# Kernel tuning notes

Hardware: AMD Instinct MI355X
Metric: run time of the kernel (lower is better)

## Reference

```python
import jax, jax.numpy as jnp
import numpy as np

N = 50000
E = 800000
D_IN = 128
D_OUT = 128


def setup_inputs() -> dict:
    key = jax.random.key(0)
    k1, k2, k3 = jax.random.split(key, 3)
    seq = jax.random.normal(k1, (N, D_IN), dtype=jnp.float32)
    edge_index = jax.random.randint(k2, (2, E), 0, N, dtype=jnp.int32)
    # Glorot-ish init for the GCNConv linear weight [in, out]
    W = jax.random.normal(k3, (D_IN, D_OUT), dtype=jnp.float32) * (1.0 / np.sqrt(D_IN))
    b = jnp.zeros((D_OUT,), dtype=jnp.float32)
    prelu_w = jnp.full((1,), 0.25, dtype=jnp.float32)
    return {"seq": seq, "edge_index": edge_index, "W": W, "b": b, "prelu_w": prelu_w}


def reference(seq, edge_index, W, b, prelu_w):
    # GCNConv: linear transform, add self-loops, symmetric normalization,
    # scatter-add aggregation, bias; then PReLU activation.
    n = seq.shape[0]
    xW = seq @ W  # [N, D_OUT]

    # add self-loops
    loop = jnp.arange(n, dtype=edge_index.dtype)
    row = jnp.concatenate([edge_index[0], loop])  # source
    col = jnp.concatenate([edge_index[1], loop])  # target

    # degree of target nodes (edge weight = 1)
    deg = jax.ops.segment_sum(jnp.ones_like(col, dtype=xW.dtype), col, num_segments=n)
    dinv = jnp.where(deg > 0, jax.lax.rsqrt(deg), 0.0)
    norm = dinv[row] * dinv[col]  # [E+N]

    msg = xW[row] * norm[:, None]  # gather + scale
    out = jax.ops.segment_sum(msg, col, num_segments=n)  # scatter-add
    out = out + b

    # PReLU with single shared weight
    return jnp.where(out > 0, out, prelu_w[0] * out)
```

## Files before the change

### kernel.cpp

```cpp
#include <hip/hip_runtime.h>

constexpr int D = 128;
constexpr int CAP = 64;
constexpr int OVFCAP = 65536;

typedef __attribute__((ext_vector_type(8))) short short8;
typedef __attribute__((ext_vector_type(4))) float f32x4;

__device__ __forceinline__ unsigned short f2bf(float f) {
    unsigned u = __float_as_uint(f);
    u += 0x7fffu + ((u >> 16) & 1u);
    return (unsigned short)(u >> 16);
}

__global__ __launch_bounds__(256) void k_prep(const float* __restrict__ W,
                                              unsigned short* __restrict__ Wf) {
    int tid = blockIdx.x * 256 + threadIdx.x;
    int j  = tid & 7;
    int l  = (tid >> 3) & 63;
    int g  = tid >> 9;
    int kc = g >> 3, t = g & 7;
    int k  = kc * 32 + ((l >> 4) * 4) + (j & 3) + ((j >> 2) * 16);
    int c  = t * 16 + (l & 15);
    Wf[tid] = f2bf(W[k * D + c]);
}

__global__ __launch_bounds__(256) void k_place_gemm(
        const int* __restrict__ row, const int* __restrict__ col,
        int* __restrict__ deg, int* __restrict__ slots,
        int* __restrict__ ovfCnt, int2* __restrict__ ovf, int E,
        int gemmBlocks,
        const float* __restrict__ seq, const unsigned short* __restrict__ Wf,
        unsigned short* __restrict__ y16, int n) {
    int b = (int)blockIdx.x;
    int half = b >> 1;
    bool isGemm = ((b & 1) == 0) && (half < gemmBlocks);

    if (!isGemm) {
        int pIdx = (b < 2 * gemmBlocks) ? half : (b - gemmBlocks);
        int t = pIdx * 256 + threadIdx.x;
        int e = 2 * t;
        if (e + 1 < E) {
            int2 c2 = *(const int2*)(col + e);
            int2 r2 = *(const int2*)(row + e);
            int p0 = atomicAdd(&deg[c2.x], 1);
            int p1 = atomicAdd(&deg[c2.y], 1);
            if (p0 < CAP) slots[(size_t)c2.x * CAP + p0] = r2.x;
            else { int o = atomicAdd(ovfCnt, 1); if (o < OVFCAP) ovf[o] = make_int2(r2.x, c2.x); }
            if (p1 < CAP) slots[(size_t)c2.y * CAP + p1] = r2.y;
            else { int o = atomicAdd(ovfCnt, 1); if (o < OVFCAP) ovf[o] = make_int2(r2.y, c2.y); }
        } else if (e < E) {
            int c = col[e];
            int r = row[e];
            int p = atomicAdd(&deg[c], 1);
            if (p < CAP) slots[(size_t)c * CAP + p] = r;
            else { int o = atomicAdd(ovfCnt, 1); if (o < OVFCAP) ovf[o] = make_int2(r, c); }
        }
        return;
    }

    int w  = threadIdx.x >> 6;
    int l  = threadIdx.x & 63;
    int lr = l & 15;
    int lg = l >> 4;

    int row0 = half * 64;
    int m = row0 + w * 16 + lr;
    if (m >= n) m = n - 1;
    const float* sp = seq + (size_t)m * D;

    f32x4 acc[8];
    #pragma unroll
    for (int t = 0; t < 8; ++t) acc[t] = (f32x4){0.f, 0.f, 0.f, 0.f};

    const short8* WfB = (const short8*)Wf;

    #pragma unroll
    for (int kc = 0; kc < 4; ++kc) {
        int kb = kc * 32 + lg * 4;
        float4 lo = *(const float4*)(sp + kb);
        float4 hi = *(const float4*)(sp + kb + 16);
        short8 a;
        a[0] = (short)f2bf(lo.x); a[1] = (short)f2bf(lo.y);
        a[2] = (short)f2bf(lo.z); a[3] = (short)f2bf(lo.w);
        a[4] = (short)f2bf(hi.x); a[5] = (short)f2bf(hi.y);
        a[6] = (short)f2bf(hi.z); a[7] = (short)f2bf(hi.w);
        #pragma unroll
        for (int t = 0; t < 8; ++t) {
            short8 bf = WfB[(kc * 8 + t) * 64 + l];
            acc[t] = __builtin_amdgcn_mfma_f32_16x16x32_bf16(a, bf, acc[t], 0, 0, 0);
        }
    }

    #pragma unroll
    for (int i = 0; i < 4; ++i) {
        int g = row0 + w * 16 + lg * 4 + i;
        if (g < n) {
            unsigned short* yp = y16 + (size_t)g * D + lr;
            #pragma unroll
            for (int t = 0; t < 8; ++t) yp[t * 16] = f2bf(acc[t][i]);
        }
    }
}

__global__ __launch_bounds__(256) void k_agg(
        const int* __restrict__ slots, const int* __restrict__ deg,
        const int* __restrict__ ovfCnt, const int2* __restrict__ ovf,
        const unsigned short* __restrict__ y16,
        const float* __restrict__ b, const float* __restrict__ pw,
        float* __restrict__ out, int n) {
    int wid = (blockIdx.x * 256 + threadIdx.x) >> 6;
    if (wid >= n) return;
    int lane = threadIdx.x & 63;

    int cntf = deg[wid];
    int cnt = cntf < CAP ? cntf : CAP;
    float dc = rsqrtf((float)(cntf + 1));

    unsigned sv = *(const unsigned*)(y16 + (size_t)wid * D + 2 * lane);
    float ax0 = __uint_as_float(sv << 16) * dc;
    float ay0 = __uint_as_float(sv & 0xffff0000u) * dc;
    float ax1 = 0.f, ay1 = 0.f, ax2 = 0.f, ay2 = 0.f, ax3 = 0.f, ay3 = 0.f;
    float ax4 = 0.f, ay4 = 0.f, ax5 = 0.f, ay5 = 0.f, ax6 = 0.f, ay6 = 0.f;
    float ax7 = 0.f, ay7 = 0.f;

    int my = (lane < cnt) ? slots[(size_t)wid * CAP + lane] : 0;

    int k = 0;
    for (; k + 7 < cnt; k += 8) {
        int r0 = __shfl(my, k);
        int r1 = __shfl(my, k + 1);
        int r2 = __shfl(my, k + 2);
        int r3 = __shfl(my, k + 3);
        int r4 = __shfl(my, k + 4);
        int r5 = __shfl(my, k + 5);
        int r6 = __shfl(my, k + 6);
        int r7 = __shfl(my, k + 7);
        int g0 = deg[r0]; int g1 = deg[r1]; int g2 = deg[r2]; int g3 = deg[r3];
        int g4 = deg[r4]; int g5 = deg[r5]; int g6 = deg[r6]; int g7 = deg[r7];
        unsigned v0 = *(const unsigned*)(y16 + (size_t)r0 * D + 2 * lane);
        unsigned v1 = *(const unsigned*)(y16 + (size_t)r1 * D + 2 * lane);
        unsigned v2 = *(const unsigned*)(y16 + (size_t)r2 * D + 2 * lane);
        unsigned v3 = *(const unsigned*)(y16 + (size_t)r3 * D + 2 * lane);
        unsigned v4 = *(const unsigned*)(y16 + (size_t)r4 * D + 2 * lane);
        unsigned v5 = *(const unsigned*)(y16 + (size_t)r5 * D + 2 * lane);
        unsigned v6 = *(const unsigned*)(y16 + (size_t)r6 * D + 2 * lane);
        unsigned v7 = *(const unsigned*)(y16 + (size_t)r7 * D + 2 * lane);
        float dr0 = rsqrtf((float)(g0 + 1));
        float dr1 = rsqrtf((float)(g1 + 1));
        float dr2 = rsqrtf((float)(g2 + 1));
        float dr3 = rsqrtf((float)(g3 + 1));
        float dr4 = rsqrtf((float)(g4 + 1));
        float dr5 = rsqrtf((float)(g5 + 1));
        float dr6 = rsqrtf((float)(g6 + 1));
        float dr7 = rsqrtf((float)(g7 + 1));
        ax0 = fmaf(__uint_as_float(v0 << 16), dr0, ax0); ay0 = fmaf(__uint_as_float(v0 & 0xffff0000u), dr0, ay0);
        ax1 = fmaf(__uint_as_float(v1 << 16), dr1, ax1); ay1 = fmaf(__uint_as_float(v1 & 0xffff0000u), dr1, ay1);
        ax2 = fmaf(__uint_as_float(v2 << 16), dr2, ax2); ay2 = fmaf(__uint_as_float(v2 & 0xffff0000u), dr2, ay2);
        ax3 = fmaf(__uint_as_float(v3 << 16), dr3, ax3); ay3 = fmaf(__uint_as_float(v3 & 0xffff0000u), dr3, ay3);
        ax4 = fmaf(__uint_as_float(v4 << 16), dr4, ax4); ay4 = fmaf(__uint_as_float(v4 & 0xffff0000u), dr4, ay4);
        ax5 = fmaf(__uint_as_float(v5 << 16), dr5, ax5); ay5 = fmaf(__uint_as_float(v5 & 0xffff0000u), dr5, ay5);
        ax6 = fmaf(__uint_as_float(v6 << 16), dr6, ax6); ay6 = fmaf(__uint_as_float(v6 & 0xffff0000u), dr6, ay6);
        ax7 = fmaf(__uint_as_float(v7 << 16), dr7, ax7); ay7 = fmaf(__uint_as_float(v7 & 0xffff0000u), dr7, ay7);
    }
    for (; k < cnt; ++k) {
        int r = __shfl(my, k);
        float dr = rsqrtf((float)(deg[r] + 1));
        unsigned v = *(const unsigned*)(y16 + (size_t)r * D + 2 * lane);
        ax0 = fmaf(__uint_as_float(v << 16), dr, ax0);
        ay0 = fmaf(__uint_as_float(v & 0xffff0000u), dr, ay0);
    }

    if (cntf > CAP) {
        int m = *ovfCnt; if (m > OVFCAP) m = OVFCAP;
        for (int j = 0; j < m; ++j) {
            int2 pr = ovf[j];
            if (pr.y == wid) {
                float dr = rsqrtf((float)(deg[pr.x] + 1));
                unsigned v = *(const unsigned*)(y16 + (size_t)pr.x * D + 2 * lane);
                ax0 = fmaf(__uint_as_float(v << 16), dr, ax0);
                ay0 = fmaf(__uint_as_float(v & 0xffff0000u), dr, ay0);
            }
        }
    }

    float sx = ((ax0 + ax1) + (ax2 + ax3)) + ((ax4 + ax5) + (ax6 + ax7));
    float sy = ((ay0 + ay1) + (ay2 + ay3)) + ((ay4 + ay5) + (ay6 + ay7));

    float2 bb = *(const float2*)(b + 2 * lane);
    float p = pw[0];
    float vx = sx * dc + bb.x;
    float vy = sy * dc + bb.y;
    vx = vx > 0.f ? vx : p * vx;
    vy = vy > 0.f ? vy : p * vy;
    *(float2*)(out + (size_t)wid * D + 2 * lane) = make_float2(vx, vy);
}

extern "C" void kernel_launch(void* const* d_in, const int* in_sizes, int n_in,
                              void* d_out, int out_size, void* d_ws, size_t ws_size,
                              hipStream_t stream) {
    const float* seq = (const float*)d_in[0];
    const int*   ei  = (const int*)d_in[1];
    const float* W   = (const float*)d_in[2];
    const float* b   = (const float*)d_in[3];
    const float* pw  = (const float*)d_in[4];
    int n = in_sizes[0] / D;
    int E = in_sizes[1] / 2;

    float* out = (float*)d_out;

    auto align = [](size_t x) { return (x + 255) & ~(size_t)255; };
    char* p = (char*)d_ws;
    unsigned short* y16 = (unsigned short*)p; p += align((size_t)n * D * sizeof(unsigned short));
    int*  deg    = (int*)p;   size_t degBytes = align((size_t)n * sizeof(int)); p += degBytes;
    int*  ovfCnt = (int*)p;   p += 256;
    int2* ovf    = (int2*)p;  p += align((size_t)OVFCAP * sizeof(int2));
    int*  slots  = (int*)p;   p += align((size_t)n * CAP * sizeof(int));
    unsigned short* Wf = (unsigned short*)p; p += align((size_t)D * D * sizeof(unsigned short));

    hipMemsetAsync(deg, 0, degBytes + 256, stream);
    k_prep<<<64, 256, 0, stream>>>(W, Wf);

    int GB = (n + 63) / 64;
    int PB = (E + 511) / 512;
    k_place_gemm<<<GB + PB, 256, 0, stream>>>(
        ei, ei + E, deg, slots, ovfCnt, ovf, E, GB, seq, Wf, y16, n);

    k_agg<<<(unsigned)(((long long)n * 64 + 255) / 256), 256, 0, stream>>>(
        slots, deg, ovfCnt, ovf, y16, b, pw, out, n);
}
```

Baseline: 99.37 us.

## Prescale features by source-degree norm and pad degree counters to cache lines

Adds a k_scale pass that multiplies each bf16 row of xW by rsqrt(deg+1) ahead of aggregation. This removes the per-neighbour degree gather and rsqrt from k_agg, whose inner loop becomes plain adds. Degree counters are padded to 64-byte stride to cut atomic contention, each placement thread handles four edges with int4 loads, and CAP drops to 48. The cost is one extra kernel launch, an extra read-write pass over y16 with a second bf16 rounding, a larger memset, and possibly more overflow traffic.

```diff
diff --git a/kernel.cpp b/kernel.cpp
--- a/kernel.cpp
+++ b/kernel.cpp
@@ -1,7 +1,8 @@
 #include <hip/hip_runtime.h>
 
 constexpr int D = 128;
-constexpr int CAP = 64;
+constexpr int CAP = 48;
+constexpr int DPAD = 16;
 constexpr int OVFCAP = 65536;
 
 typedef __attribute__((ext_vector_type(8))) short short8;
@@ -27,7 +28,7 @@
 
 __global__ __launch_bounds__(256) void k_place_gemm(
         const int* __restrict__ row, const int* __restrict__ col,
-        int* __restrict__ deg, int* __restrict__ slots,
+        int* __restrict__ degP, int* __restrict__ slots,
         int* __restrict__ ovfCnt, int2* __restrict__ ovf, int E,
         int gemmBlocks,
         const float* __restrict__ seq, const unsigned short* __restrict__ Wf,
@@ -39,22 +40,33 @@
     if (!isGemm) {
         int pIdx = (b < 2 * gemmBlocks) ? half : (b - gemmBlocks);
         int t = pIdx * 256 + threadIdx.x;
-        int e = 2 * t;
-        if (e + 1 < E) {
-            int2 c2 = *(const int2*)(col + e);
-            int2 r2 = *(const int2*)(row + e);
-            int p0 = atomicAdd(&deg[c2.x], 1);
-            int p1 = atomicAdd(&deg[c2.y], 1);
-            if (p0 < CAP) slots[(size_t)c2.x * CAP + p0] = r2.x;
-            else { int o = atomicAdd(ovfCnt, 1); if (o < OVFCAP) ovf[o] = make_int2(r2.x, c2.x); }
-            if (p1 < CAP) slots[(size_t)c2.y * CAP + p1] = r2.y;
-            else { int o = atomicAdd(ovfCnt, 1); if (o < OVFCAP) ovf[o] = make_int2(r2.y, c2.y); }
-        } else if (e < E) {
-            int c = col[e];
-            int r = row[e];
-            int p = atomicAdd(&deg[c], 1);
-            if (p < CAP) slots[(size_t)c * CAP + p] = r;
-            else { int o = atomicAdd(ovfCnt, 1); if (o < OVFCAP) ovf[o] = make_int2(r, c); }
+        int e = 4 * t;
+        if (e + 3 < E) {
+            int4 c4 = *(const int4*)(col + e);
+            int4 r4 = *(const int4*)(row + e);
+            int p0 = atomicAdd(&degP[(size_t)c4.x * DPAD], 1);
+            int p1 = atomicAdd(&degP[(size_t)c4.y * DPAD], 1);
+            int p2 = atomicAdd(&degP[(size_t)c4.z * DPAD], 1);
+            int p3 = atomicAdd(&degP[(size_t)c4.w * DPAD], 1);
+            if (p0 < CAP) slots[(size_t)c4.x * CAP + p0] = r4.x;
+            else { int o = atomicAdd(ovfCnt, 1); if (o < OVFCAP) ovf[o] = make_int2(r4.x, c4.x); }
+            if (p1 < CAP) slots[(size_t)c4.y * CAP + p1] = r4.y;
+            else { int o = atomicAdd(ovfCnt, 1); if (o < OVFCAP) ovf[o] = make_int2(r4.y, c4.y); }
+            if (p2 < CAP) slots[(size_t)c4.z * CAP + p2] = r4.z;
+            else { int o = atomicAdd(ovfCnt, 1); if (o < OVFCAP) ovf[o] = make_int2(r4.z, c4.z); }
+            if (p3 < CAP) slots[(size_t)c4.w * CAP + p3] = r4.w;
+            else { int o = atomicAdd(ovfCnt, 1); if (o < OVFCAP) ovf[o] = make_int2(r4.w, c4.w); }
+        } else {
+            for (int j = 0; j < 4; ++j) {
+                int ej = e + j;
+                if (ej < E) {
+                    int c = col[ej];
+                    int r = row[ej];
+                    int p = atomicAdd(&degP[(size_t)c * DPAD], 1);
+                    if (p < CAP) slots[(size_t)c * CAP + p] = r;
+                    else { int o = atomicAdd(ovfCnt, 1); if (o < OVFCAP) ovf[o] = make_int2(r, c); }
+                }
+            }
         }
         return;
     }
@@ -103,8 +115,40 @@
     }
 }
 
+__global__ __launch_bounds__(256) void k_scale(unsigned short* __restrict__ y16,
+                                               const int* __restrict__ degP, int n) {
+    int tid = blockIdx.x * 256 + threadIdx.x;
+    int total = n * (D / 8);
+    if (tid >= total) return;
+    int g = tid >> 4;
+    float di = rsqrtf((float)(degP[(size_t)g * DPAD] + 1));
+    uint4 v = ((uint4*)y16)[tid];
+    unsigned r0, r1, r2, r3;
+    {
+        float lo = __uint_as_float(v.x << 16) * di;
+        float hi = __uint_as_float(v.x & 0xffff0000u) * di;
+        r0 = (unsigned)f2bf(lo) | ((unsigned)f2bf(hi) << 16);
+    }
+    {
+        float lo = __uint_as_float(v.y << 16) * di;
+        float hi = __uint_as_float(v.y & 0xffff0000u) * di;
+        r1 = (unsigned)f2bf(lo) | ((unsigned)f2bf(hi) << 16);
+    }
+    {
+        float lo = __uint_as_float(v.z << 16) * di;
+        float hi = __uint_as_float(v.z & 0xffff0000u) * di;
+        r2 = (unsigned)f2bf(lo) | ((unsigned)f2bf(hi) << 16);
+    }
+    {
+        float lo = __uint_as_float(v.w << 16) * di;
+        float hi = __uint_as_float(v.w & 0xffff0000u) * di;
+        r3 = (unsigned)f2bf(lo) | ((unsigned)f2bf(hi) << 16);
+    }
+    ((uint4*)y16)[tid] = make_uint4(r0, r1, r2, r3);
+}
+
 __global__ __launch_bounds__(256) void k_agg(
-        const int* __restrict__ slots, const int* __restrict__ deg,
+        const int* __restrict__ slots, const int* __restrict__ degP,
         const int* __restrict__ ovfCnt, const int2* __restrict__ ovf,
         const unsigned short* __restrict__ y16,
         const float* __restrict__ b, const float* __restrict__ pw,
@@ -113,13 +157,13 @@
     if (wid >= n) return;
     int lane = threadIdx.x & 63;
 
-    int cntf = deg[wid];
+    int cntf = degP[(size_t)wid * DPAD];
     int cnt = cntf < CAP ? cntf : CAP;
     float dc = rsqrtf((float)(cntf + 1));
 
     unsigned sv = *(const unsigned*)(y16 + (size_t)wid * D + 2 * lane);
-    float ax0 = __uint_as_float(sv << 16) * dc;
-    float ay0 = __uint_as_float(sv & 0xffff0000u) * dc;
+    float ax0 = __uint_as_float(sv << 16);
+    float ay0 = __uint_as_float(sv & 0xffff0000u);
     float ax1 = 0.f, ay1 = 0.f, ax2 = 0.f, ay2 = 0.f, ax3 = 0.f, ay3 = 0.f;
     float ax4 = 0.f, ay4 = 0.f, ax5 = 0.f, ay5 = 0.f, ax6 = 0.f, ay6 = 0.f;
     float ax7 = 0.f, ay7 = 0.f;
@@ -136,8 +180,6 @@
         int r5 = __shfl(my, k + 5);
         int r6 = __shfl(my, k + 6);
         int r7 = __shfl(my, k + 7);
-        int g0 = deg[r0]; int g1 = deg[r1]; int g2 = deg[r2]; int g3 = deg[r3];
-        int g4 = deg[r4]; int g5 = deg[r5]; int g6 = deg[r6]; int g7 = deg[r7];
         unsigned v0 = *(const unsigned*)(y16 + (size_t)r0 * D + 2 * lane);
         unsigned v1 = *(const unsigned*)(y16 + (size_t)r1 * D + 2 * lane);
         unsigned v2 = *(const unsigned*)(y16 + (size_t)r2 * D + 2 * lane);
@@ -146,29 +188,20 @@
         unsigned v5 = *(const unsigned*)(y16 + (size_t)r5 * D + 2 * lane);
         unsigned v6 = *(const unsigned*)(y16 + (size_t)r6 * D + 2 * lane);
         unsigned v7 = *(const unsigned*)(y16 + (size_t)r7 * D + 2 * lane);
-        float dr0 = rsqrtf((float)(g0 + 1));
-        float dr1 = rsqrtf((float)(g1 + 1));
-        float dr2 = rsqrtf((float)(g2 + 1));
-        float dr3 = rsqrtf((float)(g3 + 1));
-        float dr4 = rsqrtf((float)(g4 + 1));
-        float dr5 = rsqrtf((float)(g5 + 1));
-        float dr6 = rsqrtf((float)(g6 + 1));
-        float dr7 = rsqrtf((float)(g7 + 1));
-        ax0 = fmaf(__uint_as_float(v0 << 16), dr0, ax0); ay0 = fmaf(__uint_as_float(v0 & 0xffff0000u), dr0, ay0);
-        ax1 = fmaf(__uint_as_float(v1 << 16), dr1, ax1); ay1 = fmaf(__uint_as_float(v1 & 0xffff0000u), dr1, ay1);
-        ax2 = fmaf(__uint_as_float(v2 << 16), dr2, ax2); ay2 = fmaf(__uint_as_float(v2 & 0xffff0000u), dr2, ay2);
-        ax3 = fmaf(__uint_as_float(v3 << 16), dr3, ax3); ay3 = fmaf(__uint_as_float(v3 & 0xffff0000u), dr3, ay3);
-        ax4 = fmaf(__uint_as_float(v4 << 16), dr4, ax4); ay4 = fmaf(__uint_as_float(v4 & 0xffff0000u), dr4, ay4);
-        ax5 = fmaf(__uint_as_float(v5 << 16), dr5, ax5); ay5 = fmaf(__uint_as_float(v5 & 0xffff0000u), dr5, ay5);
-        ax6 = fmaf(__uint_as_float(v6 << 16), dr6, ax6); ay6 = fmaf(__uint_as_float(v6 & 0xffff0000u), dr6, ay6);
-        ax7 = fmaf(__uint_as_float(v7 << 16), dr7, ax7); ay7 = fmaf(__uint_as_float(v7 & 0xffff0000u), dr7, ay7);
+        ax0 += __uint_as_float(v0 << 16); ay0 += __uint_as_float(v0 & 0xffff0000u);
+        ax1 += __uint_as_float(v1 << 16); ay1 += __uint_as_float(v1 & 0xffff0000u);
+        ax2 += __uint_as_float(v2 << 16); ay2 += __uint_as_float(v2 & 0xffff0000u);
+        ax3 += __uint_as_float(v3 << 16); ay3 += __uint_as_float(v3 & 0xffff0000u);
+        ax4 += __uint_as_float(v4 << 16); ay4 += __uint_as_float(v4 & 0xffff0000u);
+        ax5 += __uint_as_float(v5 << 16); ay5 += __uint_as_float(v5 & 0xffff0000u);
+        ax6 += __uint_as_float(v6 << 16); ay6 += __uint_as_float(v6 & 0xffff0000u);
+        ax7 += __uint_as_float(v7 << 16); ay7 += __uint_as_float(v7 & 0xffff0000u);
     }
     for (; k < cnt; ++k) {
         int r = __shfl(my, k);
-        float dr = rsqrtf((float)(deg[r] + 1));
         unsigned v = *(const unsigned*)(y16 + (size_t)r * D + 2 * lane);
-        ax0 = fmaf(__uint_as_float(v << 16), dr, ax0);
-        ay0 = fmaf(__uint_as_float(v & 0xffff0000u), dr, ay0);
+        ax0 += __uint_as_float(v << 16);
+        ay0 += __uint_as_float(v & 0xffff0000u);
     }
 
     if (cntf > CAP) {
@@ -176,10 +209,9 @@
         for (int j = 0; j < m; ++j) {
             int2 pr = ovf[j];
             if (pr.y == wid) {
-                float dr = rsqrtf((float)(deg[pr.x] + 1));
                 unsigned v = *(const unsigned*)(y16 + (size_t)pr.x * D + 2 * lane);
-                ax0 = fmaf(__uint_as_float(v << 16), dr, ax0);
-                ay0 = fmaf(__uint_as_float(v & 0xffff0000u), dr, ay0);
+                ax0 += __uint_as_float(v << 16);
+                ay0 += __uint_as_float(v & 0xffff0000u);
             }
         }
     }
@@ -212,20 +244,23 @@
     auto align = [](size_t x) { return (x + 255) & ~(size_t)255; };
     char* p = (char*)d_ws;
     unsigned short* y16 = (unsigned short*)p; p += align((size_t)n * D * sizeof(unsigned short));
-    int*  deg    = (int*)p;   size_t degBytes = align((size_t)n * sizeof(int)); p += degBytes;
+    int*  degP   = (int*)p;   size_t degBytes = align((size_t)n * DPAD * sizeof(int)); p += degBytes;
     int*  ovfCnt = (int*)p;   p += 256;
     int2* ovf    = (int2*)p;  p += align((size_t)OVFCAP * sizeof(int2));
     int*  slots  = (int*)p;   p += align((size_t)n * CAP * sizeof(int));
     unsigned short* Wf = (unsigned short*)p; p += align((size_t)D * D * sizeof(unsigned short));
 
-    hipMemsetAsync(deg, 0, degBytes + 256, stream);
+    hipMemsetAsync(degP, 0, degBytes + 256, stream);
     k_prep<<<64, 256, 0, stream>>>(W, Wf);
 
     int GB = (n + 63) / 64;
-    int PB = (E + 511) / 512;
+    int PB = (E + 1023) / 1024;
     k_place_gemm<<<GB + PB, 256, 0, stream>>>(
-        ei, ei + E, deg, slots, ovfCnt, ovf, E, GB, seq, Wf, y16, n);
+        ei, ei + E, degP, slots, ovfCnt, ovf, E, GB, seq, Wf, y16, n);
+
+    int scaleTotal = n * (D / 8);
+    k_scale<<<(scaleTotal + 255) / 256, 256, 0, stream>>>(y16, degP, n);
 
     k_agg<<<(unsigned)(((long long)n * 64 + 255) / 256), 256, 0, stream>>>(
-        slots, deg, ovfCnt, ovf, y16, b, pw, out, n);
-}
+        slots, degP, ovfCnt, ovf, y16, b, pw, out, n);
+}
```

Result: faster. 89.41 us (-10.0%).

## Pad degree counters, precompute dinv array, fuse zeroing into prep, shrink slot cap

Applied to the files above, without the earlier changes.

The degree counters are padded to 64-byte stride so atomics from different nodes no longer contend on shared cache lines. A new small kernel precomputes rsqrt of each degree into a dense float array, which the aggregation gathers instead of the padded counters followed by rsqrt. The memset is replaced by zeroing inside the weight-prep kernel, edge indices are read with nontemporal loads, and CAP drops from 64 to 48 to shrink the slot buffer. The costs are an extra kernel launch, a larger degree array to zero, and more edges going to the slow overflow path for high-degree nodes.

```diff
diff --git a/kernel.cpp b/kernel.cpp
--- a/kernel.cpp
+++ b/kernel.cpp
@@ -1,7 +1,8 @@
 #include <hip/hip_runtime.h>
 
 constexpr int D = 128;
-constexpr int CAP = 64;
+constexpr int CAP = 48;
+constexpr int DPAD = 16;
 constexpr int OVFCAP = 65536;
 
 typedef __attribute__((ext_vector_type(8))) short short8;
@@ -14,8 +15,11 @@
 }
 
 __global__ __launch_bounds__(256) void k_prep(const float* __restrict__ W,
-                                              unsigned short* __restrict__ Wf) {
+                                              unsigned short* __restrict__ Wf,
+                                              uint4* __restrict__ zbase, int zcnt4) {
     int tid = blockIdx.x * 256 + threadIdx.x;
+    for (int i = tid; i < zcnt4; i += 16384) zbase[i] = make_uint4(0u, 0u, 0u, 0u);
+
     int j  = tid & 7;
     int l  = (tid >> 3) & 63;
     int g  = tid >> 9;
@@ -27,7 +31,7 @@
 
 __global__ __launch_bounds__(256) void k_place_gemm(
         const int* __restrict__ row, const int* __restrict__ col,
-        int* __restrict__ deg, int* __restrict__ slots,
+        int* __restrict__ degP, int* __restrict__ slots,
         int* __restrict__ ovfCnt, int2* __restrict__ ovf, int E,
         int gemmBlocks,
         const float* __restrict__ seq, const unsigned short* __restrict__ Wf,
@@ -41,18 +45,20 @@
         int t = pIdx * 256 + threadIdx.x;
         int e = 2 * t;
         if (e + 1 < E) {
-            int2 c2 = *(const int2*)(col + e);
-            int2 r2 = *(const int2*)(row + e);
-            int p0 = atomicAdd(&deg[c2.x], 1);
-            int p1 = atomicAdd(&deg[c2.y], 1);
-            if (p0 < CAP) slots[(size_t)c2.x * CAP + p0] = r2.x;
-            else { int o = atomicAdd(ovfCnt, 1); if (o < OVFCAP) ovf[o] = make_int2(r2.x, c2.x); }
-            if (p1 < CAP) slots[(size_t)c2.y * CAP + p1] = r2.y;
-            else { int o = atomicAdd(ovfCnt, 1); if (o < OVFCAP) ovf[o] = make_int2(r2.y, c2.y); }
+            unsigned long long cc = __builtin_nontemporal_load((const unsigned long long*)(col + e));
+            unsigned long long rr = __builtin_nontemporal_load((const unsigned long long*)(row + e));
+            int c0 = (int)(cc & 0xffffffffu), c1 = (int)(cc >> 32);
+            int r0 = (int)(rr & 0xffffffffu), r1 = (int)(rr >> 32);
+            int p0 = atomicAdd(&degP[(size_t)c0 * DPAD], 1);
+            int p1 = atomicAdd(&degP[(size_t)c1 * DPAD], 1);
+            if (p0 < CAP) slots[(size_t)c0 * CAP + p0] = r0;
+            else { int o = atomicAdd(ovfCnt, 1); if (o < OVFCAP) ovf[o] = make_int2(r0, c0); }
+            if (p1 < CAP) slots[(size_t)c1 * CAP + p1] = r1;
+            else { int o = atomicAdd(ovfCnt, 1); if (o < OVFCAP) ovf[o] = make_int2(r1, c1); }
         } else if (e < E) {
             int c = col[e];
             int r = row[e];
-            int p = atomicAdd(&deg[c], 1);
+            int p = atomicAdd(&degP[(size_t)c * DPAD], 1);
             if (p < CAP) slots[(size_t)c * CAP + p] = r;
             else { int o = atomicAdd(ovfCnt, 1); if (o < OVFCAP) ovf[o] = make_int2(r, c); }
         }
@@ -103,8 +109,15 @@
     }
 }
 
+__global__ __launch_bounds__(256) void k_dinv(const int* __restrict__ degP,
+                                              float* __restrict__ dinv, int n) {
+    int i = blockIdx.x * 256 + threadIdx.x;
+    if (i < n) dinv[i] = rsqrtf((float)(degP[(size_t)i * DPAD] + 1));
+}
+
 __global__ __launch_bounds__(256) void k_agg(
-        const int* __restrict__ slots, const int* __restrict__ deg,
+        const int* __restrict__ slots, const int* __restrict__ degP,
+        const float* __restrict__ dinv,
         const int* __restrict__ ovfCnt, const int2* __restrict__ ovf,
         const unsigned short* __restrict__ y16,
         const float* __restrict__ b, const float* __restrict__ pw,
@@ -113,9 +126,9 @@
     if (wid >= n) return;
     int lane = threadIdx.x & 63;
 
-    int cntf = deg[wid];
+    int cntf = degP[(size_t)wid * DPAD];
     int cnt = cntf < CAP ? cntf : CAP;
-    float dc = rsqrtf((float)(cntf + 1));
+    float dc = dinv[wid];
 
     unsigned sv = *(const unsigned*)(y16 + (size_t)wid * D + 2 * lane);
     float ax0 = __uint_as_float(sv << 16) * dc;
@@ -136,8 +149,8 @@
         int r5 = __shfl(my, k + 5);
         int r6 = __shfl(my, k + 6);
         int r7 = __shfl(my, k + 7);
-        int g0 = deg[r0]; int g1 = deg[r1]; int g2 = deg[r2]; int g3 = deg[r3];
-        int g4 = deg[r4]; int g5 = deg[r5]; int g6 = deg[r6]; int g7 = deg[r7];
+        float d0 = dinv[r0]; float d1 = dinv[r1]; float d2 = dinv[r2]; float d3 = dinv[r3];
+        float d4 = dinv[r4]; float d5 = dinv[r5]; float d6 = dinv[r6]; float d7 = dinv[r7];
         unsigned v0 = *(const unsigned*)(y16 + (size_t)r0 * D + 2 * lane);
         unsigned v1 = *(const unsigned*)(y16 + (size_t)r1 * D + 2 * lane);
         unsigned v2 = *(const unsigned*)(y16 + (size_t)r2 * D + 2 * lane);
@@ -146,26 +159,18 @@
         unsigned v5 = *(const unsigned*)(y16 + (size_t)r5 * D + 2 * lane);
         unsigned v6 = *(const unsigned*)(y16 + (size_t)r6 * D + 2 * lane);
         unsigned v7 = *(const unsigned*)(y16 + (size_t)r7 * D + 2 * lane);
-        float dr0 = rsqrtf((float)(g0 + 1));
-        float dr1 = rsqrtf((float)(g1 + 1));
-        float dr2 = rsqrtf((float)(g2 + 1));
-        float dr3 = rsqrtf((float)(g3 + 1));
-        float dr4 = rsqrtf((float)(g4 + 1));
-        float dr5 = rsqrtf((float)(g5 + 1));
-        float dr6 = rsqrtf((float)(g6 + 1));
-        float dr7 = rsqrtf((float)(g7 + 1));
-        ax0 = fmaf(__uint_as_float(v0 << 16), dr0, ax0); ay0 = fmaf(__uint_as_float(v0 & 0xffff0000u), dr0, ay0);
-        ax1 = fmaf(__uint_as_float(v1 << 16), dr1, ax1); ay1 = fmaf(__uint_as_float(v1 & 0xffff0000u), dr1, ay1);
-        ax2 = fmaf(__uint_as_float(v2 << 16), dr2, ax2); ay2 = fmaf(__uint_as_float(v2 & 0xffff0000u), dr2, ay2);
-        ax3 = fmaf(__uint_as_float(v3 << 16), dr3, ax3); ay3 = fmaf(__uint_as_float(v3 & 0xffff0000u), dr3, ay3);
-        ax4 = fmaf(__uint_as_float(v4 << 16), dr4, ax4); ay4 = fmaf(__uint_as_float(v4 & 0xffff0000u), dr4, ay4);
-        ax5 = fmaf(__uint_as_float(v5 << 16), dr5, ax5); ay5 = fmaf(__uint_as_float(v5 & 0xffff0000u), dr5, ay5);
-        ax6 = fmaf(__uint_as_float(v6 << 16), dr6, ax6); ay6 = fmaf(__uint_as_float(v6 & 0xffff0000u), dr6, ay6);
-        ax7 = fmaf(__uint_as_float(v7 << 16), dr7, ax7); ay7 = fmaf(__uint_as_float(v7 & 0xffff0000u), dr7, ay7);
+        ax0 = fmaf(__uint_as_float(v0 << 16), d0, ax0); ay0 = fmaf(__uint_as_float(v0 & 0xffff0000u), d0, ay0);
+        ax1 = fmaf(__uint_as_float(v1 << 16), d1, ax1); ay1 = fmaf(__uint_as_float(v1 & 0xffff0000u), d1, ay1);
+        ax2 = fmaf(__uint_as_float(v2 << 16), d2, ax2); ay2 = fmaf(__uint_as_float(v2 & 0xffff0000u), d2, ay2);
+        ax3 = fmaf(__uint_as_float(v3 << 16), d3, ax3); ay3 = fmaf(__uint_as_float(v3 & 0xffff0000u), d3, ay3);
+        ax4 = fmaf(__uint_as_float(v4 << 16), d4, ax4); ay4 = fmaf(__uint_as_float(v4 & 0xffff0000u), d4, ay4);
+        ax5 = fmaf(__uint_as_float(v5 << 16), d5, ax5); ay5 = fmaf(__uint_as_float(v5 & 0xffff0000u), d5, ay5);
+        ax6 = fmaf(__uint_as_float(v6 << 16), d6, ax6); ay6 = fmaf(__uint_as_float(v6 & 0xffff0000u), d6, ay6);
+        ax7 = fmaf(__uint_as_float(v7 << 16), d7, ax7); ay7 = fmaf(__uint_as_float(v7 & 0xffff0000u), d7, ay7);
     }
     for (; k < cnt; ++k) {
         int r = __shfl(my, k);
-        float dr = rsqrtf((float)(deg[r] + 1));
+        float dr = dinv[r];
         unsigned v = *(const unsigned*)(y16 + (size_t)r * D + 2 * lane);
         ax0 = fmaf(__uint_as_float(v << 16), dr, ax0);
         ay0 = fmaf(__uint_as_float(v & 0xffff0000u), dr, ay0);
@@ -176,7 +181,7 @@
         for (int j = 0; j < m; ++j) {
             int2 pr = ovf[j];
             if (pr.y == wid) {
-                float dr = rsqrtf((float)(deg[pr.x] + 1));
+                float dr = dinv[pr.x];
                 unsigned v = *(const unsigned*)(y16 + (size_t)pr.x * D + 2 * lane);
                 ax0 = fmaf(__uint_as_float(v << 16), dr, ax0);
                 ay0 = fmaf(__uint_as_float(v & 0xffff0000u), dr, ay0);
@@ -212,20 +217,23 @@
     auto align = [](size_t x) { return (x + 255) & ~(size_t)255; };
     char* p = (char*)d_ws;
     unsigned short* y16 = (unsigned short*)p; p += align((size_t)n * D * sizeof(unsigned short));
-    int*  deg    = (int*)p;   size_t degBytes = align((size_t)n * sizeof(int)); p += degBytes;
+    int*  degP   = (int*)p;   size_t degBytes = align((size_t)n * DPAD * sizeof(int)); p += degBytes;
     int*  ovfCnt = (int*)p;   p += 256;
     int2* ovf    = (int2*)p;  p += align((size_t)OVFCAP * sizeof(int2));
     int*  slots  = (int*)p;   p += align((size_t)n * CAP * sizeof(int));
     unsigned short* Wf = (unsigned short*)p; p += align((size_t)D * D * sizeof(unsigned short));
-
-    hipMemsetAsync(deg, 0, degBytes + 256, stream);
-    k_prep<<<64, 256, 0, stream>>>(W, Wf);
+    float* dinv  = (float*)p; p += align((size_t)n * sizeof(float));
+
+    int zcnt4 = (int)((degBytes + 256) / 16);
+    k_prep<<<64, 256, 0, stream>>>(W, Wf, (uint4*)degP, zcnt4);
 
     int GB = (n + 63) / 64;
     int PB = (E + 511) / 512;
     k_place_gemm<<<GB + PB, 256, 0, stream>>>(
-        ei, ei + E, deg, slots, ovfCnt, ovf, E, GB, seq, Wf, y16, n);
+        ei, ei + E, degP, slots, ovfCnt, ovf, E, GB, seq, Wf, y16, n);
+
+    k_dinv<<<(n + 255) / 256, 256, 0, stream>>>(degP, dinv, n);
 
     k_agg<<<(unsigned)(((long long)n * 64 + 255) / 256), 256, 0, stream>>>(
-        slots, deg, ovfCnt, ovf, y16, b, pw, out, n);
-}
+        slots, degP, dinv, ovfCnt, ovf, y16, b, pw, out, n);
+}
```

Result: no change. 101.2 us (+1.9%).

## Pad degree counters, fold memset into prep kernel, process four edges per thread

Applied to the files above, without the earlier changes.

Each node's degree counter now sits on its own 64-byte slot (stride 16 ints) to reduce atomic contention on shared cache lines. The separate memset is replaced by a zeroing loop inside the prep kernel, the placement threads each handle four edges with int4 loads, and the slot capacity drops from 64 to 48. The tradeoffs are a 16x larger degree array to zero (about 3.2MB) and scattered 64-byte-strided reads of degree in the aggregation kernel, which reduce cache locality.

```diff
diff --git a/kernel.cpp b/kernel.cpp
--- a/kernel.cpp
+++ b/kernel.cpp
@@ -1,7 +1,8 @@
 #include <hip/hip_runtime.h>
 
 constexpr int D = 128;
-constexpr int CAP = 64;
+constexpr int CAP = 48;
+constexpr int DPAD = 16;
 constexpr int OVFCAP = 65536;
 
 typedef __attribute__((ext_vector_type(8))) short short8;
@@ -14,8 +15,11 @@
 }
 
 __global__ __launch_bounds__(256) void k_prep(const float* __restrict__ W,
-                                              unsigned short* __restrict__ Wf) {
+                                              unsigned short* __restrict__ Wf,
+                                              uint4* __restrict__ zbase, int zcnt4) {
     int tid = blockIdx.x * 256 + threadIdx.x;
+    for (int i = tid; i < zcnt4; i += 16384) zbase[i] = make_uint4(0u, 0u, 0u, 0u);
+
     int j  = tid & 7;
     int l  = (tid >> 3) & 63;
     int g  = tid >> 9;
@@ -27,7 +31,7 @@
 
 __global__ __launch_bounds__(256) void k_place_gemm(
         const int* __restrict__ row, const int* __restrict__ col,
-        int* __restrict__ deg, int* __restrict__ slots,
+        int* __restrict__ degP, int* __restrict__ slots,
         int* __restrict__ ovfCnt, int2* __restrict__ ovf, int E,
         int gemmBlocks,
         const float* __restrict__ seq, const unsigned short* __restrict__ Wf,
@@ -39,22 +43,33 @@
     if (!isGemm) {
         int pIdx = (b < 2 * gemmBlocks) ? half : (b - gemmBlocks);
         int t = pIdx * 256 + threadIdx.x;
-        int e = 2 * t;
-        if (e + 1 < E) {
-            int2 c2 = *(const int2*)(col + e);
-            int2 r2 = *(const int2*)(row + e);
-            int p0 = atomicAdd(&deg[c2.x], 1);
-            int p1 = atomicAdd(&deg[c2.y], 1);
-            if (p0 < CAP) slots[(size_t)c2.x * CAP + p0] = r2.x;
-            else { int o = atomicAdd(ovfCnt, 1); if (o < OVFCAP) ovf[o] = make_int2(r2.x, c2.x); }
-            if (p1 < CAP) slots[(size_t)c2.y * CAP + p1] = r2.y;
-            else { int o = atomicAdd(ovfCnt, 1); if (o < OVFCAP) ovf[o] = make_int2(r2.y, c2.y); }
-        } else if (e < E) {
-            int c = col[e];
-            int r = row[e];
-            int p = atomicAdd(&deg[c], 1);
-            if (p < CAP) slots[(size_t)c * CAP + p] = r;
-            else { int o = atomicAdd(ovfCnt, 1); if (o < OVFCAP) ovf[o] = make_int2(r, c); }
+        int e = 4 * t;
+        if (e + 3 < E) {
+            int4 c4 = *(const int4*)(col + e);
+            int4 r4 = *(const int4*)(row + e);
+            int p0 = atomicAdd(&degP[(size_t)c4.x * DPAD], 1);
+            int p1 = atomicAdd(&degP[(size_t)c4.y * DPAD], 1);
+            int p2 = atomicAdd(&degP[(size_t)c4.z * DPAD], 1);
+            int p3 = atomicAdd(&degP[(size_t)c4.w * DPAD], 1);
+            if (p0 < CAP) slots[(size_t)c4.x * CAP + p0] = r4.x;
+            else { int o = atomicAdd(ovfCnt, 1); if (o < OVFCAP) ovf[o] = make_int2(r4.x, c4.x); }
+            if (p1 < CAP) slots[(size_t)c4.y * CAP + p1] = r4.y;
+            else { int o = atomicAdd(ovfCnt, 1); if (o < OVFCAP) ovf[o] = make_int2(r4.y, c4.y); }
+            if (p2 < CAP) slots[(size_t)c4.z * CAP + p2] = r4.z;
+            else { int o = atomicAdd(ovfCnt, 1); if (o < OVFCAP) ovf[o] = make_int2(r4.z, c4.z); }
+            if (p3 < CAP) slots[(size_t)c4.w * CAP + p3] = r4.w;
+            else { int o = atomicAdd(ovfCnt, 1); if (o < OVFCAP) ovf[o] = make_int2(r4.w, c4.w); }
+        } else {
+            for (int j = 0; j < 4; ++j) {
+                int ej = e + j;
+                if (ej < E) {
+                    int c = col[ej];
+                    int r = row[ej];
+                    int p = atomicAdd(&degP[(size_t)c * DPAD], 1);
+                    if (p < CAP) slots[(size_t)c * CAP + p] = r;
+                    else { int o = atomicAdd(ovfCnt, 1); if (o < OVFCAP) ovf[o] = make_int2(r, c); }
+                }
+            }
         }
         return;
     }
@@ -104,7 +119,7 @@
 }
 
 __global__ __launch_bounds__(256) void k_agg(
-        const int* __restrict__ slots, const int* __restrict__ deg,
+        const int* __restrict__ slots, const int* __restrict__ degP,
         const int* __restrict__ ovfCnt, const int2* __restrict__ ovf,
         const unsigned short* __restrict__ y16,
         const float* __restrict__ b, const float* __restrict__ pw,
@@ -113,7 +128,7 @@
     if (wid >= n) return;
     int lane = threadIdx.x & 63;
 
-    int cntf = deg[wid];
+    int cntf = degP[(size_t)wid * DPAD];
     int cnt = cntf < CAP ? cntf : CAP;
     float dc = rsqrtf((float)(cntf + 1));
 
@@ -136,8 +151,10 @@
         int r5 = __shfl(my, k + 5);
         int r6 = __shfl(my, k + 6);
         int r7 = __shfl(my, k + 7);
-        int g0 = deg[r0]; int g1 = deg[r1]; int g2 = deg[r2]; int g3 = deg[r3];
-        int g4 = deg[r4]; int g5 = deg[r5]; int g6 = deg[r6]; int g7 = deg[r7];
+        int g0 = degP[(size_t)r0 * DPAD]; int g1 = degP[(size_t)r1 * DPAD];
+        int g2 = degP[(size_t)r2 * DPAD]; int g3 = degP[(size_t)r3 * DPAD];
+        int g4 = degP[(size_t)r4 * DPAD]; int g5 = degP[(size_t)r5 * DPAD];
+        int g6 = degP[(size_t)r6 * DPAD]; int g7 = degP[(size_t)r7 * DPAD];
         unsigned v0 = *(const unsigned*)(y16 + (size_t)r0 * D + 2 * lane);
         unsigned v1 = *(const unsigned*)(y16 + (size_t)r1 * D + 2 * lane);
         unsigned v2 = *(const unsigned*)(y16 + (size_t)r2 * D + 2 * lane);
@@ -165,7 +182,7 @@
     }
     for (; k < cnt; ++k) {
         int r = __shfl(my, k);
-        float dr = rsqrtf((float)(deg[r] + 1));
+        float dr = rsqrtf((float)(degP[(size_t)r * DPAD] + 1));
         unsigned v = *(const unsigned*)(y16 + (size_t)r * D + 2 * lane);
         ax0 = fmaf(__uint_as_float(v << 16), dr, ax0);
         ay0 = fmaf(__uint_as_float(v & 0xffff0000u), dr, ay0);
@@ -176,7 +193,7 @@
         for (int j = 0; j < m; ++j) {
             int2 pr = ovf[j];
             if (pr.y == wid) {
-                float dr = rsqrtf((float)(deg[pr.x] + 1));
+                float dr = rsqrtf((float)(degP[(size_t)pr.x * DPAD] + 1));
                 unsigned v = *(const unsigned*)(y16 + (size_t)pr.x * D + 2 * lane);
                 ax0 = fmaf(__uint_as_float(v << 16), dr, ax0);
                 ay0 = fmaf(__uint_as_float(v & 0xffff0000u), dr, ay0);
@@ -212,20 +229,20 @@
     auto align = [](size_t x) { return (x + 255) & ~(size_t)255; };
     char* p = (char*)d_ws;
     unsigned short* y16 = (unsigned short*)p; p += align((size_t)n * D * sizeof(unsigned short));
-    int*  deg    = (int*)p;   size_t degBytes = align((size_t)n * sizeof(int)); p += degBytes;
+    int*  degP   = (int*)p;   size_t degBytes = align((size_t)n * DPAD * sizeof(int)); p += degBytes;
     int*  ovfCnt = (int*)p;   p += 256;
     int2* ovf    = (int2*)p;  p += align((size_t)OVFCAP * sizeof(int2));
     int*  slots  = (int*)p;   p += align((size_t)n * CAP * sizeof(int));
     unsigned short* Wf = (unsigned short*)p; p += align((size_t)D * D * sizeof(unsigned short));
 
-    hipMemsetAsync(deg, 0, degBytes + 256, stream);
-    k_prep<<<64, 256, 0, stream>>>(W, Wf);
+    int zcnt4 = (int)((degBytes + 256) / 16);
+    k_prep<<<64, 256, 0, stream>>>(W, Wf, (uint4*)degP, zcnt4);
 
     int GB = (n + 63) / 64;
-    int PB = (E + 511) / 512;
+    int PB = (E + 1023) / 1024;
     k_place_gemm<<<GB + PB, 256, 0, stream>>>(
-        ei, ei + E, deg, slots, ovfCnt, ovf, E, GB, seq, Wf, y16, n);
+        ei, ei + E, degP, slots, ovfCnt, ovf, E, GB, seq, Wf, y16, n);
 
     k_agg<<<(unsigned)(((long long)n * 64 + 255) / 256), 256, 0, stream>>>(
-        slots, deg, ovfCnt, ovf, y16, b, pw, out, n);
-}
+        slots, degP, ovfCnt, ovf, y16, b, pw, out, n);
+}
```

Result: faster. 94.84 us (-4.6%).
